# Kernel tuning notes

Measured on AMD Instinct MI355X. Metric: run time of the kernel, lower is better.

The kernel has to match this reference:

```python
import jax, jax.numpy as jnp
import numpy as np

N = 100000   # nodes
E = 1600000  # edges
G = 64       # graphs in batch
F_IN = 128
H = 128
SV = 64
AD = 32


def setup_inputs() -> dict:
    key = jax.random.key(0)
    ks = jax.random.split(key, 12)
    s = 0.05
    return {
        "x": jax.random.normal(ks[0], (N, F_IN), jnp.float32),
        "edge_index": jax.random.randint(ks[1], (2, E), 0, N, dtype=jnp.int64),
        "batch": jnp.sort(jax.random.randint(ks[2], (N,), 0, G, dtype=jnp.int64)),
        "state_vector": jax.random.normal(ks[3], (G, SV), jnp.float32),
        "action": jax.random.normal(ks[4], (G, AD), jnp.float32),
        "W1": jax.random.normal(ks[5], (F_IN, H), jnp.float32) * s,
        "b1": jnp.zeros((H,), jnp.float32),
        "W2": jax.random.normal(ks[6], (H, H), jnp.float32) * s,
        "b2": jnp.zeros((H,), jnp.float32),
        "Wf1": jax.random.normal(ks[7], (H + SV + AD, 256), jnp.float32) * s,
        "bf1": jnp.zeros((256,), jnp.float32),
        "Wf2": jax.random.normal(ks[8], (256, 256), jnp.float32) * s,
        "bf2": jnp.zeros((256,), jnp.float32),
        "Wo": jax.random.normal(ks[9], (256, 1), jnp.float32) * s,
        "bo": jnp.zeros((1,), jnp.float32),
    }


def gcn_conv(x, W, b, src, dst, deg_inv_sqrt):
    # PyG GCNConv: h = x @ W; aggregate D^-1/2 (A+I) D^-1/2 h; + b
    h = x @ W
    norm = deg_inv_sqrt[src] * deg_inv_sqrt[dst]          # [E]
    agg = jax.ops.segment_sum(h[src] * norm[:, None], dst, num_segments=N)
    agg = agg + h * (deg_inv_sqrt * deg_inv_sqrt)[:, None]  # self loops
    return agg + b


def reference(x, edge_index, batch, state_vector, action,
              W1, b1, W2, b2, Wf1, bf1, Wf2, bf2, Wo, bo):
    src, dst = edge_index[0], edge_index[1]
    # degree after adding self loops (aggregation index = dst, PyG default flow)
    deg = jax.ops.segment_sum(jnp.ones((E,), jnp.float32), dst, num_segments=N) + 1.0
    deg_inv_sqrt = jax.lax.rsqrt(deg)

    h = jax.nn.relu(gcn_conv(x, W1, b1, src, dst, deg_inv_sqrt))
    h = jax.nn.relu(gcn_conv(h, W2, b2, src, dst, deg_inv_sqrt))

    # global_mean_pool over graph ids
    sums = jax.ops.segment_sum(h, batch, num_segments=G)
    cnts = jax.ops.segment_sum(jnp.ones((N,), jnp.float32), batch, num_segments=G)
    pooled = sums / jnp.maximum(cnts, 1.0)[:, None]       # [G, H]

    z = jnp.concatenate([pooled, state_vector, action], axis=1)  # [G, H+SV+AD]
    z = jax.nn.relu(z @ Wf1 + bf1)
    z = jax.nn.relu(z @ Wf2 + bf2)
    return z @ Wo + bo                                     # [G, 1]
```

## Files before the change

### kernel.cpp

```cpp
#include <hip/hip_runtime.h>
#include <hip/hip_bf16.h>
#include <stdint.h>

#define N_NODES 100000
#define N_EDGES 1600000
#define N_GRAPHS 64
#define HDIM 128

#define BUCKET_SHIFT 9
#define NBUCK ((N_NODES + 511) >> 9)
#define CAP 9216
#define SCAT_CHUNK 8192
#define SCAT_NBLK ((N_EDGES + SCAT_CHUNK - 1) / SCAT_CHUNK)
#define GB_NBLK ((N_NODES + 255) / 256)

typedef __bf16 bf16x8 __attribute__((ext_vector_type(8)));
typedef float f32x4 __attribute__((ext_vector_type(4)));
typedef float f32x2 __attribute__((ext_vector_type(2)));

__global__ __launch_bounds__(256) void setup_kernel(const int* __restrict__ batch,
                                                    int* __restrict__ gstart,
                                                    const float* __restrict__ W1,
                                                    const float* __restrict__ W2,
                                                    __hip_bfloat16* __restrict__ Wt1,
                                                    __hip_bfloat16* __restrict__ Wt2,
                                                    int* __restrict__ gcur,
                                                    float* __restrict__ psum) {
    int bid = blockIdx.x;
    if (bid < GB_NBLK) {
        int i = bid * 256 + threadIdx.x;
        if (i >= N_NODES) return;
        int b = batch[i];
        int prev = (i == 0) ? -1 : batch[i - 1];
        for (int g = prev + 1; g <= b; ++g) gstart[g] = i;
        if (i == N_NODES - 1) {
            for (int g = b + 1; g <= N_GRAPHS; ++g) gstart[g] = N_NODES;
        }
    } else if (bid < GB_NBLK + 128) {
        int t = bid - GB_NBLK;
        const float* W = (t < 64) ? W1 : W2;
        __hip_bfloat16* Wt = (t < 64) ? Wt1 : Wt2;
        int bb = t & 63;
        int n = bb * 2 + (threadIdx.x >> 7);
        int k = threadIdx.x & 127;
        Wt[n * 128 + k] = __float2bfloat16(W[k * 128 + n]);
    } else {
        int i = (bid - GB_NBLK - 128) * 256 + threadIdx.x;
        if (i < NBUCK) gcur[i] = i * CAP;
        int j = i - NBUCK;
        if (j >= 0 && j < N_GRAPHS * HDIM) psum[j] = 0.f;
    }
}
#define SETUP_NBLK (GB_NBLK + 128 + (NBUCK + N_GRAPHS * HDIM + 255) / 256)

__global__ __launch_bounds__(256) void scatter_kernel(const int* __restrict__ src,
                                                      const int* __restrict__ dst,
                                                      int* __restrict__ gcur,
                                                      int* __restrict__ sorted, int E) {
    __shared__ int hist[NBUCK];
    __shared__ int base_s[NBUCK];
    int tid = threadIdx.x;
    int e0 = blockIdx.x * SCAT_CHUNK;
    int sv[SCAT_CHUNK / 256], dv[SCAT_CHUNK / 256];
#pragma unroll
    for (int j = 0; j < SCAT_CHUNK / 256; j++) {
        int e = e0 + (j << 8) + tid;
        if (e < E) { sv[j] = src[e]; dv[j] = dst[e]; } else { sv[j] = -1; dv[j] = -1; }
    }
    if (tid < NBUCK) hist[tid] = 0;
    __syncthreads();
#pragma unroll
    for (int j = 0; j < SCAT_CHUNK / 256; j++)
        if (dv[j] >= 0) atomicAdd(&hist[dv[j] >> BUCKET_SHIFT], 1);
    __syncthreads();
    if (tid < NBUCK) {
        int c = hist[tid];
        base_s[tid] = (c > 0) ? atomicAdd(&gcur[tid], c) : 0;
    }
    __syncthreads();
    if (tid < NBUCK) hist[tid] = 0;
    __syncthreads();
#pragma unroll
    for (int j = 0; j < SCAT_CHUNK / 256; j++) {
        if (dv[j] >= 0) {
            int b = dv[j] >> BUCKET_SHIFT;
            int idx = atomicAdd(&hist[b], 1);
            sorted[base_s[b] + idx] = ((dv[j] & 511) << 17) | sv[j];
        }
    }
}

__global__ __launch_bounds__(256) void bucket_build_kernel(const int* __restrict__ sorted,
                                                           const int* __restrict__ gcur,
                                                           int2* __restrict__ rs2,
                                                           float* __restrict__ dis,
                                                           int* __restrict__ csr_src) {
    __shared__ int edges[CAP];
    __shared__ int cnt[512];
    __shared__ int excl[512];
    __shared__ int ps[256];
    int b = blockIdx.x, tid = threadIdx.x;
    cnt[tid] = 0; cnt[tid + 256] = 0;
    int node0 = b << BUCKET_SHIFT;
    int lo = b * CAP, hi = gcur[b];
    int ne = hi - lo;
    for (int i = tid; i < ne; i += 256) edges[i] = sorted[lo + i];
    __syncthreads();
    for (int i = tid; i < ne; i += 256)
        atomicAdd(&cnt[((unsigned)edges[i]) >> 17], 1);
    __syncthreads();
    int c0 = cnt[2 * tid], c1 = cnt[2 * tid + 1];
    ps[tid] = c0 + c1;
    __syncthreads();
#pragma unroll
    for (int off = 1; off < 256; off <<= 1) {
        int t = (tid >= off) ? ps[tid - off] : 0;
        __syncthreads();
        ps[tid] += t;
        __syncthreads();
    }
    int pex = ps[tid] - (c0 + c1);
    excl[2 * tid] = pex;
    excl[2 * tid + 1] = pex + c0;
    __syncthreads();
#pragma unroll
    for (int k = 0; k < 2; k++) {
        int li = tid + k * 256;
        int node = node0 + li;
        if (node < N_NODES) {
            int st = lo + excl[li];
            int c = cnt[li];
            rs2[node] = make_int2(st, st + c);
            dis[node] = rsqrtf((float)c + 1.0f);
        }
    }
    cnt[tid] = 0; cnt[tid + 256] = 0;
    __syncthreads();
    for (int i = tid; i < ne; i += 256) {
        int v = edges[i];
        int li = ((unsigned)v) >> 17;
        int idx = atomicAdd(&cnt[li], 1);
        csr_src[lo + excl[li] + idx] = v & 0x1FFFF;
    }
}

template<bool A_FP32>
__global__ __launch_bounds__(256) void gemm_mfma_kernel(const void* __restrict__ Av,
                                                        const __hip_bfloat16* __restrict__ Wt,
                                                        const float* __restrict__ scale,
                                                        unsigned char* __restrict__ C, int nrows) {
    __shared__ float Cs[64 * 132];
    int tid = threadIdx.x;
    int wave = tid >> 6, lane = tid & 63;
    int quad = lane >> 4, l16 = lane & 15;
    int row0 = blockIdx.x * 64;
    int arow = row0 + wave * 16 + l16;
    int arow_c = min(arow, nrows - 1);

    const __hip_bfloat16* A16 = (const __hip_bfloat16*)Av;
    const float* A32 = (const float*)Av;

    f32x4 acc[8];
#pragma unroll
    for (int t = 0; t < 8; t++) acc[t] = (f32x4){0.f, 0.f, 0.f, 0.f};

#pragma unroll
    for (int kt = 0; kt < 4; kt++) {
        int kbase = kt * 32 + quad * 8;
        union { bf16x8 v; __hip_bfloat16 h[8]; uint4 u; } au;
        if (A_FP32) {
            const float* ap = A32 + (size_t)arow_c * 128 + kbase;
            float4 u0 = *(const float4*)ap;
            float4 u1 = *(const float4*)(ap + 4);
            au.h[0] = __float2bfloat16(u0.x); au.h[1] = __float2bfloat16(u0.y);
            au.h[2] = __float2bfloat16(u0.z); au.h[3] = __float2bfloat16(u0.w);
            au.h[4] = __float2bfloat16(u1.x); au.h[5] = __float2bfloat16(u1.y);
            au.h[6] = __float2bfloat16(u1.z); au.h[7] = __float2bfloat16(u1.w);
        } else {
            au.u = *(const uint4*)(A16 + (size_t)arow_c * 128 + kbase);
        }
#pragma unroll
        for (int t = 0; t < 8; t++) {
            bf16x8 b = *(const bf16x8*)(Wt + (size_t)(t * 16 + l16) * 128 + kbase);
            acc[t] = __builtin_amdgcn_mfma_f32_16x16x32_bf16(au.v, b, acc[t], 0, 0, 0);
        }
    }

    int rbase = wave * 16 + quad * 4;
    float s[4];
#pragma unroll
    for (int r = 0; r < 4; r++) s[r] = scale[min(row0 + rbase + r, nrows - 1)];
#pragma unroll
    for (int t = 0; t < 8; t++) {
#pragma unroll
        for (int r = 0; r < 4; r++)
            Cs[(rbase + r) * 132 + t * 16 + l16] = acc[t][r] * s[r];
    }
    __syncthreads();

#pragma unroll
    for (int p = 0; p < 4; p++) {
        int g = p * 256 + tid;
        int row = g >> 4, c8 = (g & 15) * 8;
        int grow = row0 + row;
        if (grow < nrows) {
            const float* cp = &Cs[row * 132 + c8];
            float4 v0 = *(const float4*)cp;
            float4 v1 = *(const float4*)(cp + 4);
            int w0 = __builtin_amdgcn_cvt_pk_fp8_f32(v0.x, v0.y, 0, false);
            w0 = __builtin_amdgcn_cvt_pk_fp8_f32(v0.z, v0.w, w0, true);
            int w1 = __builtin_amdgcn_cvt_pk_fp8_f32(v1.x, v1.y, 0, false);
            w1 = __builtin_amdgcn_cvt_pk_fp8_f32(v1.z, v1.w, w1, true);
            *(uint2*)(C + (size_t)grow * 128 + c8) = make_uint2((unsigned)w0, (unsigned)w1);
        }
    }
}

__device__ __forceinline__ void accum8(float* acc, uint2 u) {
    f32x2 d0 = __builtin_amdgcn_cvt_pk_f32_fp8((int)u.x, false);
    f32x2 d1 = __builtin_amdgcn_cvt_pk_f32_fp8((int)u.x, true);
    f32x2 d2 = __builtin_amdgcn_cvt_pk_f32_fp8((int)u.y, false);
    f32x2 d3 = __builtin_amdgcn_cvt_pk_f32_fp8((int)u.y, true);
    acc[0] += d0[0]; acc[1] += d0[1]; acc[2] += d1[0]; acc[3] += d1[1];
    acc[4] += d2[0]; acc[5] += d2[1]; acc[6] += d3[0]; acc[7] += d3[1];
}

__global__ __launch_bounds__(256) void agg_kernel(const unsigned char* __restrict__ h8,
                                                  const float* __restrict__ dis,
                                                  const int2* __restrict__ rs2,
                                                  const int* __restrict__ csr_src,
                                                  const float* __restrict__ bias,
                                                  __hip_bfloat16* __restrict__ out, int n) {
    int node = blockIdx.x * 4 + (threadIdx.x >> 6);
    if (node >= n) return;
    int lane = threadIdx.x & 63;
    int q = lane >> 4, f = lane & 15;
    float acc[8];
#pragma unroll
    for (int j = 0; j < 8; j++) acc[j] = 0.f;
    int2 se = rs2[node];
    int i = se.x, i1 = se.y;
    for (; i + 8 <= i1; i += 8) {
        int s0 = csr_src[i + q];
        int s1 = csr_src[i + 4 + q];
        uint2 u0 = *(const uint2*)(h8 + (size_t)s0 * 128 + f * 8);
        uint2 u1 = *(const uint2*)(h8 + (size_t)s1 * 128 + f * 8);
        accum8(acc, u0);
        accum8(acc, u1);
    }
    for (; i + 4 <= i1; i += 4) {
        int s = csr_src[i + q];
        uint2 u = *(const uint2*)(h8 + (size_t)s * 128 + f * 8);
        accum8(acc, u);
    }
    if (i < i1) {
        bool valid = (i + q) < i1;
        int e = valid ? (i + q) : (i1 - 1);
        int s = csr_src[e];
        uint2 u = *(const uint2*)(h8 + (size_t)s * 128 + f * 8);
        if (valid) accum8(acc, u);
    }
    if (q == 0) {
        uint2 u = *(const uint2*)(h8 + (size_t)node * 128 + f * 8);
        accum8(acc, u);
    }
#pragma unroll
    for (int j = 0; j < 8; j++) {
        float v = acc[j];
        v += __shfl_down(v, 32, 64);
        v += __shfl_down(v, 16, 64);
        acc[j] = v;
    }
    if (q == 0) {
        float dn = dis[node];
        float4 b0 = *(const float4*)(bias + f * 8);
        float4 b1 = *(const float4*)(bias + f * 8 + 4);
        float r0 = fmaxf(fmaf(acc[0], dn, b0.x), 0.f);
        float r1 = fmaxf(fmaf(acc[1], dn, b0.y), 0.f);
        float r2 = fmaxf(fmaf(acc[2], dn, b0.z), 0.f);
        float r3 = fmaxf(fmaf(acc[3], dn, b0.w), 0.f);
        float r4 = fmaxf(fmaf(acc[4], dn, b1.x), 0.f);
        float r5 = fmaxf(fmaf(acc[5], dn, b1.y), 0.f);
        float r6 = fmaxf(fmaf(acc[6], dn, b1.z), 0.f);
        float r7 = fmaxf(fmaf(acc[7], dn, b1.w), 0.f);
        __hip_bfloat162 p0 = __float22bfloat162_rn(make_float2(r0, r1));
        __hip_bfloat162 p1 = __float22bfloat162_rn(make_float2(r2, r3));
        __hip_bfloat162 p2 = __float22bfloat162_rn(make_float2(r4, r5));
        __hip_bfloat162 p3 = __float22bfloat162_rn(make_float2(r6, r7));
        uint4 pk;
        pk.x = *(unsigned int*)&p0; pk.y = *(unsigned int*)&p1;
        pk.z = *(unsigned int*)&p2; pk.w = *(unsigned int*)&p3;
        *(uint4*)(out + (size_t)node * 128 + f * 8) = pk;
    }
}

#define POOL_ROWS 128
__global__ __launch_bounds__(256) void pool_kernel(const __hip_bfloat16* __restrict__ h,
                                                   const int* __restrict__ batch,
                                                   const int* __restrict__ gstart,
                                                   float* __restrict__ psum, int n) {
    __shared__ float red[16 * 128];
    int tid = threadIdx.x;
    int rr = tid >> 4, fg = tid & 15;
    int r0 = blockIdx.x * POOL_ROWS;
    if (r0 >= n) return;
    int r1 = min(n, r0 + POOL_ROWS);
    int g = batch[r0];
    int seg_lo = r0;
    while (seg_lo < r1) {
        while (gstart[g + 1] <= seg_lo) g++;
        int seg_hi = min(r1, gstart[g + 1]);
        float a[8];
#pragma unroll
        for (int j = 0; j < 8; j++) a[j] = 0.f;
        for (int r = seg_lo + rr; r < seg_hi; r += 16) {
            uint4 u = *(const uint4*)(h + (size_t)r * 128 + fg * 8);
            float2 f0 = __bfloat1622float2(*(__hip_bfloat162*)&u.x);
            float2 f1 = __bfloat1622float2(*(__hip_bfloat162*)&u.y);
            float2 f2 = __bfloat1622float2(*(__hip_bfloat162*)&u.z);
            float2 f3 = __bfloat1622float2(*(__hip_bfloat162*)&u.w);
            a[0] += f0.x; a[1] += f0.y; a[2] += f1.x; a[3] += f1.y;
            a[4] += f2.x; a[5] += f2.y; a[6] += f3.x; a[7] += f3.y;
        }
        *(float4*)&red[rr * 128 + fg * 8] = make_float4(a[0], a[1], a[2], a[3]);
        *(float4*)&red[rr * 128 + fg * 8 + 4] = make_float4(a[4], a[5], a[6], a[7]);
        __syncthreads();
        if (tid < 128) {
            float s = 0.f;
#pragma unroll
            for (int k = 0; k < 16; k++) s += red[k * 128 + tid];
            atomicAdd(&psum[g * 128 + tid], s);
        }
        __syncthreads();
        seg_lo = seg_hi;
    }
}

__global__ __launch_bounds__(256) void mlp_kernel(const float* __restrict__ psum,
                                                  const int* __restrict__ gstart,
                                                  const float* __restrict__ sv,
                                                  const float* __restrict__ act,
                                                  const float* __restrict__ Wf1,
                                                  const float* __restrict__ bf1,
                                                  const float* __restrict__ Wf2,
                                                  const float* __restrict__ bf2,
                                                  const float* __restrict__ Wo,
                                                  const float* __restrict__ bo,
                                                  float* __restrict__ out) {
    int g = blockIdx.x, tid = threadIdx.x;
    __shared__ float z[224];
    __shared__ float z1[256];
    __shared__ float red[256];
    if (tid < 128) {
        int c = gstart[g + 1] - gstart[g];
        float cnt = fmaxf((float)c, 1.f);
        z[tid] = psum[g * 128 + tid] / cnt;
    } else if (tid < 192) {
        z[tid] = sv[g * 64 + (tid - 128)];
    } else if (tid < 224) {
        z[tid] = act[g * 32 + (tid - 192)];
    }
    __syncthreads();
    float a = bf1[tid];
    for (int k = 0; k < 224; k++) a = fmaf(z[k], Wf1[k * 256 + tid], a);
    z1[tid] = fmaxf(a, 0.f);
    __syncthreads();
    float b = bf2[tid];
    for (int k = 0; k < 256; k++) b = fmaf(z1[k], Wf2[k * 256 + tid], b);
    b = fmaxf(b, 0.f);
    red[tid] = b * Wo[tid];
    __syncthreads();
    for (int off = 128; off > 0; off >>= 1) {
        if (tid < off) red[tid] += red[tid + off];
        __syncthreads();
    }
    if (tid == 0) out[g] = red[0] + bo[0];
}

extern "C" void kernel_launch(void* const* d_in, const int* in_sizes, int n_in,
                              void* d_out, int out_size, void* d_ws, size_t ws_size,
                              hipStream_t stream) {
    const float* x   = (const float*)d_in[0];
    const int*   eidx = (const int*)d_in[1];
    const int*   batch = (const int*)d_in[2];
    const float* sv  = (const float*)d_in[3];
    const float* act = (const float*)d_in[4];
    const float* W1  = (const float*)d_in[5];
    const float* b1  = (const float*)d_in[6];
    const float* W2  = (const float*)d_in[7];
    const float* b2  = (const float*)d_in[8];
    const float* Wf1 = (const float*)d_in[9];
    const float* bf1 = (const float*)d_in[10];
    const float* Wf2 = (const float*)d_in[11];
    const float* bf2 = (const float*)d_in[12];
    const float* Wo  = (const float*)d_in[13];
    const float* bo  = (const float*)d_in[14];
    float* out = (float*)d_out;

    const int* srcp = eidx;
    const int* dstp = eidx + N_EDGES;

    char* w = (char*)d_ws;
    int* gcur = (int*)w;               w += (size_t)NBUCK * 4;
    float* psum = (float*)w;           w += (size_t)N_GRAPHS * HDIM * 4;
    int2* rs2 = (int2*)w;              w += (size_t)N_NODES * 8;
    float* dis = (float*)w;            w += (size_t)N_NODES * 4;
    int* gstart = (int*)w;             w += (size_t)(N_GRAPHS + 1) * 4;
    w = (char*)(((uintptr_t)w + 255) & ~(uintptr_t)255);
    int* csr_src = (int*)w;            w += (size_t)NBUCK * CAP * 4;
    w = (char*)(((uintptr_t)w + 255) & ~(uintptr_t)255);
    int* sorted = (int*)w;             w += (size_t)NBUCK * CAP * 4;
    w = (char*)(((uintptr_t)w + 255) & ~(uintptr_t)255);
    __hip_bfloat16* Wt1 = (__hip_bfloat16*)w;   w += (size_t)HDIM * HDIM * 2;
    __hip_bfloat16* Wt2 = (__hip_bfloat16*)w;   w += (size_t)HDIM * HDIM * 2;
    w = (char*)(((uintptr_t)w + 255) & ~(uintptr_t)255);
    unsigned char* hbuf = (unsigned char*)w;    w += (size_t)N_NODES * HDIM;
    w = (char*)(((uintptr_t)w + 255) & ~(uintptr_t)255);
    __hip_bfloat16* abuf = (__hip_bfloat16*)w;  w += (size_t)N_NODES * HDIM * 2;

    setup_kernel<<<SETUP_NBLK, 256, 0, stream>>>(batch, gstart, W1, W2, Wt1, Wt2, gcur, psum);

    scatter_kernel<<<SCAT_NBLK, 256, 0, stream>>>(srcp, dstp, gcur, sorted, N_EDGES);
    bucket_build_kernel<<<NBUCK, 256, 0, stream>>>(sorted, gcur, rs2, dis, csr_src);

    int gemm_blocks = (N_NODES + 63) / 64;
    int agg_blocks = (N_NODES + 3) / 4;

    gemm_mfma_kernel<true><<<gemm_blocks, 256, 0, stream>>>(x, Wt1, dis, hbuf, N_NODES);
    agg_kernel<<<agg_blocks, 256, 0, stream>>>(hbuf, dis, rs2, csr_src, b1, abuf, N_NODES);
    gemm_mfma_kernel<false><<<gemm_blocks, 256, 0, stream>>>(abuf, Wt2, dis, hbuf, N_NODES);
    agg_kernel<<<agg_blocks, 256, 0, stream>>>(hbuf, dis, rs2, csr_src, b2, abuf, N_NODES);

    pool_kernel<<<(N_NODES + POOL_ROWS - 1) / POOL_ROWS, 256, 0, stream>>>(abuf, batch, gstart, psum, N_NODES);
    mlp_kernel<<<N_GRAPHS, 256, 0, stream>>>(psum, gstart, sv, act, Wf1, bf1, Wf2, bf2, Wo, bo, out);
}
```

Measured before the change: 330.6 us.

## Split each wave across two nodes and fold self-loops into CSR

The aggregation kernel now gives each half-wave its own destination node, so a wave handles two nodes instead of one. Each half loads up to 32 neighbor indices in one coalesced read and broadcasts them with shuffles, and each wave issues four row gathers per iteration. The CSR build appends the node itself as an extra edge so the self-loop needs no separate branch, and the bucket capacity grows to fit the extra entries. Accumulation uses packed float2 adds. The aim is better lane utilization and fewer dependent index loads, at the cost of imbalance when the two nodes in a wave have different degrees.

```diff
diff --git a/kernel.cpp b/kernel.cpp
--- a/kernel.cpp
+++ b/kernel.cpp
@@ -9,7 +9,7 @@
 
 #define BUCKET_SHIFT 9
 #define NBUCK ((N_NODES + 511) >> 9)
-#define CAP 9216
+#define CAP 9728
 #define SCAT_CHUNK 8192
 #define SCAT_NBLK ((N_EDGES + SCAT_CHUNK - 1) / SCAT_CHUNK)
 #define GB_NBLK ((N_NODES + 255) / 256)
@@ -128,10 +128,11 @@
         int li = tid + k * 256;
         int node = node0 + li;
         if (node < N_NODES) {
-            int st = lo + excl[li];
+            int st = lo + excl[li] + li;
             int c = cnt[li];
-            rs2[node] = make_int2(st, st + c);
+            rs2[node] = make_int2(st, st + c + 1);
             dis[node] = rsqrtf((float)c + 1.0f);
+            csr_src[st + c] = node;
         }
     }
     cnt[tid] = 0; cnt[tid + 256] = 0;
@@ -140,7 +141,7 @@
         int v = edges[i];
         int li = ((unsigned)v) >> 17;
         int idx = atomicAdd(&cnt[li], 1);
-        csr_src[lo + excl[li] + idx] = v & 0x1FFFF;
+        csr_src[lo + excl[li] + li + idx] = v & 0x1FFFF;
     }
 }
 
@@ -216,13 +217,11 @@
     }
 }
 
-__device__ __forceinline__ void accum8(float* acc, uint2 u) {
-    f32x2 d0 = __builtin_amdgcn_cvt_pk_f32_fp8((int)u.x, false);
-    f32x2 d1 = __builtin_amdgcn_cvt_pk_f32_fp8((int)u.x, true);
-    f32x2 d2 = __builtin_amdgcn_cvt_pk_f32_fp8((int)u.y, false);
-    f32x2 d3 = __builtin_amdgcn_cvt_pk_f32_fp8((int)u.y, true);
-    acc[0] += d0[0]; acc[1] += d0[1]; acc[2] += d1[0]; acc[3] += d1[1];
-    acc[4] += d2[0]; acc[5] += d2[1]; acc[6] += d3[0]; acc[7] += d3[1];
+__device__ __forceinline__ void accum8p(f32x2* acc, uint2 u) {
+    acc[0] += __builtin_amdgcn_cvt_pk_f32_fp8((int)u.x, false);
+    acc[1] += __builtin_amdgcn_cvt_pk_f32_fp8((int)u.x, true);
+    acc[2] += __builtin_amdgcn_cvt_pk_f32_fp8((int)u.y, false);
+    acc[3] += __builtin_amdgcn_cvt_pk_f32_fp8((int)u.y, true);
 }
 
 __global__ __launch_bounds__(256) void agg_kernel(const unsigned char* __restrict__ h8,
@@ -231,58 +230,77 @@
                                                   const int* __restrict__ csr_src,
                                                   const float* __restrict__ bias,
                                                   __hip_bfloat16* __restrict__ out, int n) {
-    int node = blockIdx.x * 4 + (threadIdx.x >> 6);
-    if (node >= n) return;
+    int wid = threadIdx.x >> 6;
     int lane = threadIdx.x & 63;
-    int q = lane >> 4, f = lane & 15;
-    float acc[8];
-#pragma unroll
-    for (int j = 0; j < 8; j++) acc[j] = 0.f;
-    int2 se = rs2[node];
-    int i = se.x, i1 = se.y;
-    for (; i + 8 <= i1; i += 8) {
-        int s0 = csr_src[i + q];
-        int s1 = csr_src[i + 4 + q];
-        uint2 u0 = *(const uint2*)(h8 + (size_t)s0 * 128 + f * 8);
-        uint2 u1 = *(const uint2*)(h8 + (size_t)s1 * 128 + f * 8);
-        accum8(acc, u0);
-        accum8(acc, u1);
-    }
-    for (; i + 4 <= i1; i += 4) {
-        int s = csr_src[i + q];
-        uint2 u = *(const uint2*)(h8 + (size_t)s * 128 + f * 8);
-        accum8(acc, u);
-    }
-    if (i < i1) {
-        bool valid = (i + q) < i1;
-        int e = valid ? (i + q) : (i1 - 1);
-        int s = csr_src[e];
-        uint2 u = *(const uint2*)(h8 + (size_t)s * 128 + f * 8);
-        if (valid) accum8(acc, u);
-    }
-    if (q == 0) {
-        uint2 u = *(const uint2*)(h8 + (size_t)node * 128 + f * 8);
-        accum8(acc, u);
-    }
-#pragma unroll
-    for (int j = 0; j < 8; j++) {
-        float v = acc[j];
-        v += __shfl_down(v, 32, 64);
-        v += __shfl_down(v, 16, 64);
+    int half = lane >> 5;
+    int q = lane >> 4;
+    int f = lane & 15;
+    int l32 = lane & 31;
+    int sub = q & 1;
+    int hb = half << 5;
+
+    int nodeA = blockIdx.x * 8 + wid * 2;
+    if (nodeA >= n) return;
+    int nodeB = nodeA + 1;
+    bool hasB = nodeB < n;
+    int myNode = half ? (hasB ? nodeB : nodeA) : nodeA;
+
+    int2 se = rs2[myNode];
+    int i0 = se.x;
+    int deg = se.y - se.x;
+    if (half && !hasB) deg = 0;
+
+    float dn = dis[myNode];
+    float4 b0 = *(const float4*)(bias + f * 8);
+    float4 b1 = *(const float4*)(bias + f * 8 + 4);
+
+    f32x2 acc[4];
+#pragma unroll
+    for (int j = 0; j < 4; j++) acc[j] = (f32x2){0.f, 0.f};
+
+    for (int base = 0; base < deg; base += 32) {
+        int cnt = min(deg - base, 32);
+        int idx = csr_src[i0 + base + min(l32, cnt - 1)];
+        int e = 0;
+        for (; e + 8 <= cnt; e += 8) {
+            int s0 = __shfl(idx, hb + e + sub, 64);
+            int s1 = __shfl(idx, hb + e + 2 + sub, 64);
+            int s2 = __shfl(idx, hb + e + 4 + sub, 64);
+            int s3 = __shfl(idx, hb + e + 6 + sub, 64);
+            uint2 u0 = *(const uint2*)(h8 + (size_t)s0 * 128 + f * 8);
+            uint2 u1 = *(const uint2*)(h8 + (size_t)s1 * 128 + f * 8);
+            uint2 u2 = *(const uint2*)(h8 + (size_t)s2 * 128 + f * 8);
+            uint2 u3 = *(const uint2*)(h8 + (size_t)s3 * 128 + f * 8);
+            accum8p(acc, u0);
+            accum8p(acc, u1);
+            accum8p(acc, u2);
+            accum8p(acc, u3);
+        }
+        for (; e < cnt; e += 2) {
+            bool valid = (e + sub) < cnt;
+            int s = __shfl(idx, hb + min(e + sub, cnt - 1), 64);
+            uint2 u = *(const uint2*)(h8 + (size_t)s * 128 + f * 8);
+            if (valid) accum8p(acc, u);
+        }
+    }
+
+#pragma unroll
+    for (int j = 0; j < 4; j++) {
+        f32x2 v = acc[j];
+        v[0] += __shfl_down(v[0], 16, 64);
+        v[1] += __shfl_down(v[1], 16, 64);
         acc[j] = v;
     }
-    if (q == 0) {
-        float dn = dis[node];
-        float4 b0 = *(const float4*)(bias + f * 8);
-        float4 b1 = *(const float4*)(bias + f * 8 + 4);
-        float r0 = fmaxf(fmaf(acc[0], dn, b0.x), 0.f);
-        float r1 = fmaxf(fmaf(acc[1], dn, b0.y), 0.f);
-        float r2 = fmaxf(fmaf(acc[2], dn, b0.z), 0.f);
-        float r3 = fmaxf(fmaf(acc[3], dn, b0.w), 0.f);
-        float r4 = fmaxf(fmaf(acc[4], dn, b1.x), 0.f);
-        float r5 = fmaxf(fmaf(acc[5], dn, b1.y), 0.f);
-        float r6 = fmaxf(fmaf(acc[6], dn, b1.z), 0.f);
-        float r7 = fmaxf(fmaf(acc[7], dn, b1.w), 0.f);
+
+    if (sub == 0 && (half == 0 || hasB)) {
+        float r0 = fmaxf(fmaf(acc[0][0], dn, b0.x), 0.f);
+        float r1 = fmaxf(fmaf(acc[0][1], dn, b0.y), 0.f);
+        float r2 = fmaxf(fmaf(acc[1][0], dn, b0.z), 0.f);
+        float r3 = fmaxf(fmaf(acc[1][1], dn, b0.w), 0.f);
+        float r4 = fmaxf(fmaf(acc[2][0], dn, b1.x), 0.f);
+        float r5 = fmaxf(fmaf(acc[2][1], dn, b1.y), 0.f);
+        float r6 = fmaxf(fmaf(acc[3][0], dn, b1.z), 0.f);
+        float r7 = fmaxf(fmaf(acc[3][1], dn, b1.w), 0.f);
         __hip_bfloat162 p0 = __float22bfloat162_rn(make_float2(r0, r1));
         __hip_bfloat162 p1 = __float22bfloat162_rn(make_float2(r2, r3));
         __hip_bfloat162 p2 = __float22bfloat162_rn(make_float2(r4, r5));
@@ -290,7 +308,7 @@
         uint4 pk;
         pk.x = *(unsigned int*)&p0; pk.y = *(unsigned int*)&p1;
         pk.z = *(unsigned int*)&p2; pk.w = *(unsigned int*)&p3;
-        *(uint4*)(out + (size_t)node * 128 + f * 8) = pk;
+        *(uint4*)(out + (size_t)myNode * 128 + f * 8) = pk;
     }
 }
 
@@ -424,7 +442,7 @@
     bucket_build_kernel<<<NBUCK, 256, 0, stream>>>(sorted, gcur, rs2, dis, csr_src);
 
     int gemm_blocks = (N_NODES + 63) / 64;
-    int agg_blocks = (N_NODES + 3) / 4;
+    int agg_blocks = (N_NODES + 7) / 8;
 
     gemm_mfma_kernel<true><<<gemm_blocks, 256, 0, stream>>>(x, Wt1, dis, hbuf, N_NODES);
     agg_kernel<<<agg_blocks, 256, 0, stream>>>(hbuf, dis, rs2, csr_src, b1, abuf, N_NODES);
```

Measured after the change: 296.3 us. 10.4% less time.
